# Performance work log

Hardware: AMD Instinct MI355X
Metric: run time of the kernel (lower is better)

Reference implementation:

```python
import jax, jax.numpy as jnp
import numpy as np

NEG_SLOPE = 0.01  # torch nn.LeakyReLU default


def setup_inputs() -> dict:
    key = jax.random.key(0)
    k1, k2, k3, k4 = jax.random.split(key, 4)
    B, N, d = 256, 64, 64
    embeddings = jax.random.normal(k1, (B, N, d), dtype=jnp.float32)
    # nn.Linear(em_dim, em_dim): weight [d, d] (out, in), bias [d]
    w_W = jax.random.normal(k2, (d, d), dtype=jnp.float32) / np.sqrt(d)
    w_b = jax.random.normal(k3, (d,), dtype=jnp.float32) * 0.01
    # nn.Linear(em_dim, 1): weight [1, d] -> stored as [d], bias [1]
    a_W = jax.random.normal(k4, (d,), dtype=jnp.float32) / np.sqrt(d)
    a_b = jnp.zeros((1,), dtype=jnp.float32)
    return {"embeddings": embeddings, "w_W": w_W, "w_b": w_b, "a_W": a_W, "a_b": a_b}


def reference(embeddings, w_W, w_b, a_W, a_b):
    # pairwise elementwise product: value[b,i,j,d] = emb[b,i,d] * emb[b,j,d]
    value = embeddings[:, :, None, :] * embeddings[:, None, :, :]  # [B,N,N,d]
    # small linear d->d (torch Linear: x @ W.T + b)
    qk = jnp.einsum('bijd,ed->bije', value, w_W) + w_b
    qk = jnp.where(qk >= 0, qk, NEG_SLOPE * qk)  # LeakyReLU
    # dropout is identity in eval mode
    logits = jnp.einsum('bijd,d->bij', qk, a_W) + a_b[0]  # linear d->1, squeeze
    alphas = jax.nn.softmax(logits, axis=-1)[..., None]  # [B,N,N,1]
    return alphas, value
```

## Files before the change

kernel.cpp:

```cpp
#include <hip/hip_runtime.h>

typedef __attribute__((ext_vector_type(8))) short short8;
typedef __attribute__((ext_vector_type(4))) float floatx4;
typedef __attribute__((ext_vector_type(4))) int   intx4;

#define NEG_SLOPE 0.01f

__device__ __forceinline__ short f2bf(float f) {
    unsigned u = __float_as_uint(f);
    unsigned r = (u + 0x7FFFu + ((u >> 16) & 1u)) >> 16;
    return (short)r;
}

__device__ __forceinline__ int pack2(float x, float y) {
    return (int)(unsigned short)f2bf(x) | ((int)(unsigned short)f2bf(y) << 16);
}

__global__ __launch_bounds__(512, 4)
void afm_kernel(const float* __restrict__ emb,
                const float* __restrict__ wW,
                const float* __restrict__ wb,
                const float* __restrict__ aW,
                float* __restrict__ aOut,
                float* __restrict__ vOut) {
    __shared__ __align__(16) float sEf[64][68];
    __shared__ __align__(16) float sW [64][68];
    __shared__ __align__(16) short sEb[64][72];
    __shared__ __align__(16) float sei[8][64];
    __shared__ __align__(16) float swb[64];
    __shared__ __align__(16) float saw[64];
    __shared__ __align__(16) float slog[8][64];

    const int tid   = threadIdx.x;
    const int lane  = tid & 63;
    const int w     = tid >> 6;
    const int blk   = blockIdx.x;
    const int b     = blk >> 3;
    const int iBase = (blk & 7) << 3;
    const int i     = iBase + w;

    const float* embB = emb + (size_t)b * 4096;

    {
        int row = tid >> 3;
        int c0  = (tid & 7) << 3;
        const float* src = embB + row * 64 + c0;
        float4 a0 = *(const float4*)(src);
        float4 a1 = *(const float4*)(src + 4);
        *(float4*)&sEf[row][c0]     = a0;
        *(float4*)&sEf[row][c0 + 4] = a1;
        intx4 q;
        q[0] = pack2(a0.x, a0.y); q[1] = pack2(a0.z, a0.w);
        q[2] = pack2(a1.x, a1.y); q[3] = pack2(a1.z, a1.w);
        *(intx4*)&sEb[row][c0] = q;

        const float* wsrc = wW + row * 64 + c0;
        float4 b0 = *(const float4*)(wsrc);
        float4 b1 = *(const float4*)(wsrc + 4);
        *(float4*)&sW[row][c0]     = b0;
        *(float4*)&sW[row][c0 + 4] = b1;

        sei[w][lane] = embB[i * 64 + lane];
        if (tid < 64)        swb[tid]       = wb[tid];
        else if (tid < 128)  saw[tid - 64]  = aW[tid - 64];
    }
    __syncthreads();

    {
        float* base = vOut + ((size_t)(b * 64 + i) << 12);
        const int joff = lane >> 4;
        const int d0   = (lane & 15) << 2;
        float4 ei = *(float4*)&sei[w][d0];
        #pragma unroll
        for (int c = 0; c < 16; ++c) {
            int j = (c << 2) + joff;
            float4 ej = *(float4*)&sEf[j][d0];
            floatx4 v;
            v[0] = ei.x * ej.x; v[1] = ei.y * ej.y;
            v[2] = ei.z * ej.z; v[3] = ei.w * ej.w;
            __builtin_nontemporal_store(v, (floatx4*)(base + (c << 8) + (lane << 2)));
        }
    }

    const int lo = lane & 15, hi = lane >> 4;

    short8 bf[2][4];
    #pragma unroll
    for (int kt = 0; kt < 2; ++kt) {
        const int d0 = kt * 32 + hi * 8;
        float4 ei0 = *(float4*)&sei[w][d0];
        float4 ei1 = *(float4*)&sei[w][d0 + 4];
        #pragma unroll
        for (int et = 0; et < 4; ++et) {
            int e = et * 16 + lo;
            float4 w0 = *(float4*)&sW[e][d0];
            float4 w1 = *(float4*)&sW[e][d0 + 4];
            short8 t;
            t[0] = f2bf(w0.x * ei0.x); t[1] = f2bf(w0.y * ei0.y);
            t[2] = f2bf(w0.z * ei0.z); t[3] = f2bf(w0.w * ei0.w);
            t[4] = f2bf(w1.x * ei1.x); t[5] = f2bf(w1.y * ei1.y);
            t[6] = f2bf(w1.z * ei1.z); t[7] = f2bf(w1.w * ei1.w);
            bf[kt][et] = t;
        }
    }

    float wbv[4], awv[4];
    #pragma unroll
    for (int et = 0; et < 4; ++et) {
        int e = et * 16 + lo;
        wbv[et] = swb[e];
        awv[et] = saw[e];
    }

    float lg[16];
    #pragma unroll
    for (int jt = 0; jt < 4; ++jt) {
        floatx4 acc[4];
        #pragma unroll
        for (int et = 0; et < 4; ++et)
            acc[et] = (floatx4){0.f, 0.f, 0.f, 0.f};
        #pragma unroll
        for (int kt = 0; kt < 2; ++kt) {
            short8 af = *(short8*)&sEb[jt * 16 + lo][kt * 32 + hi * 8];
            #pragma unroll
            for (int et = 0; et < 4; ++et)
                acc[et] = __builtin_amdgcn_mfma_f32_16x16x32_bf16(
                    af, bf[kt][et], acc[et], 0, 0, 0);
        }
        #pragma unroll
        for (int r = 0; r < 4; ++r) {
            float p = 0.f;
            #pragma unroll
            for (int et = 0; et < 4; ++et) {
                float x = acc[et][r] + wbv[et];
                x = fmaxf(x, NEG_SLOPE * x);
                p += awv[et] * x;
            }
            p += __shfl_xor(p, 1);
            p += __shfl_xor(p, 2);
            p += __shfl_xor(p, 4);
            p += __shfl_xor(p, 8);
            lg[jt * 4 + r] = p;
        }
    }

    float m = lg[0];
    #pragma unroll
    for (int k = 1; k < 16; ++k) m = fmaxf(m, lg[k]);
    m = fmaxf(m, __shfl_xor(m, 16));
    m = fmaxf(m, __shfl_xor(m, 32));

    float ex[16];
    float s = 0.f;
    #pragma unroll
    for (int k = 0; k < 16; ++k) { ex[k] = __expf(lg[k] - m); s += ex[k]; }
    s += __shfl_xor(s, 16);
    s += __shfl_xor(s, 32);
    float inv = 1.f / s;

    if (lo == 0) {
        #pragma unroll
        for (int jt = 0; jt < 4; ++jt)
            #pragma unroll
            for (int r = 0; r < 4; ++r)
                slog[w][jt * 16 + hi * 4 + r] = ex[jt * 4 + r] * inv;
    }
    __syncthreads();
    aOut[((size_t)(b * 64 + i) << 6) + lane] = slog[w][lane];
}

extern "C" void kernel_launch(void* const* d_in, const int* in_sizes, int n_in,
                              void* d_out, int out_size, void* d_ws, size_t ws_size,
                              hipStream_t stream) {
    const float* emb = (const float*)d_in[0];
    const float* wW  = (const float*)d_in[1];
    const float* wb  = (const float*)d_in[2];
    const float* aW  = (const float*)d_in[3];
    float* aOut = (float*)d_out;
    float* vOut = aOut + (size_t)256 * 64 * 64;
    afm_kernel<<<2048, 512, 0, stream>>>(emb, wW, wb, aW, aOut, vOut);
}
```

Measured before the change: 279.5 us.

## Interleave value stores with MFMA logit compute and drop weight staging in LDS

Moves the value-tensor nontemporal stores into the same loop as the MFMA logit computation, so each group of four store chunks is followed by one jt tile of matrix work, overlapping the write stream with compute. Weight, bias and attention vectors are now read directly from global memory instead of being staged through shared memory, which shrinks the LDS footprint. The final block-wide __syncthreads is replaced with a wave barrier, since each wave only reads its own slog row. Logits pass through shared memory so the softmax can read them back, at the cost of an extra LDS round trip and redundant per-thread global weight loads.

```diff
diff --git a/kernel.cpp b/kernel.cpp
--- a/kernel.cpp
+++ b/kernel.cpp
@@ -24,11 +24,8 @@
                 float* __restrict__ aOut,
                 float* __restrict__ vOut) {
     __shared__ __align__(16) float sEf[64][68];
-    __shared__ __align__(16) float sW [64][68];
     __shared__ __align__(16) short sEb[64][72];
     __shared__ __align__(16) float sei[8][64];
-    __shared__ __align__(16) float swb[64];
-    __shared__ __align__(16) float saw[64];
     __shared__ __align__(16) float slog[8][64];
 
     const int tid   = threadIdx.x;
@@ -54,33 +51,9 @@
         q[2] = pack2(a1.x, a1.y); q[3] = pack2(a1.z, a1.w);
         *(intx4*)&sEb[row][c0] = q;
 
-        const float* wsrc = wW + row * 64 + c0;
-        float4 b0 = *(const float4*)(wsrc);
-        float4 b1 = *(const float4*)(wsrc + 4);
-        *(float4*)&sW[row][c0]     = b0;
-        *(float4*)&sW[row][c0 + 4] = b1;
-
         sei[w][lane] = embB[i * 64 + lane];
-        if (tid < 64)        swb[tid]       = wb[tid];
-        else if (tid < 128)  saw[tid - 64]  = aW[tid - 64];
     }
     __syncthreads();
-
-    {
-        float* base = vOut + ((size_t)(b * 64 + i) << 12);
-        const int joff = lane >> 4;
-        const int d0   = (lane & 15) << 2;
-        float4 ei = *(float4*)&sei[w][d0];
-        #pragma unroll
-        for (int c = 0; c < 16; ++c) {
-            int j = (c << 2) + joff;
-            float4 ej = *(float4*)&sEf[j][d0];
-            floatx4 v;
-            v[0] = ei.x * ej.x; v[1] = ei.y * ej.y;
-            v[2] = ei.z * ej.z; v[3] = ei.w * ej.w;
-            __builtin_nontemporal_store(v, (floatx4*)(base + (c << 8) + (lane << 2)));
-        }
-    }
 
     const int lo = lane & 15, hi = lane >> 4;
 
@@ -92,9 +65,9 @@
         float4 ei1 = *(float4*)&sei[w][d0 + 4];
         #pragma unroll
         for (int et = 0; et < 4; ++et) {
-            int e = et * 16 + lo;
-            float4 w0 = *(float4*)&sW[e][d0];
-            float4 w1 = *(float4*)&sW[e][d0 + 4];
+            const float* wp = wW + (et * 16 + lo) * 64 + d0;
+            float4 w0 = *(const float4*)(wp);
+            float4 w1 = *(const float4*)(wp + 4);
             short8 t;
             t[0] = f2bf(w0.x * ei0.x); t[1] = f2bf(w0.y * ei0.y);
             t[2] = f2bf(w0.z * ei0.z); t[3] = f2bf(w0.w * ei0.w);
@@ -103,57 +76,85 @@
             bf[kt][et] = t;
         }
     }
-
     float wbv[4], awv[4];
     #pragma unroll
     for (int et = 0; et < 4; ++et) {
-        int e = et * 16 + lo;
-        wbv[et] = swb[e];
-        awv[et] = saw[e];
+        wbv[et] = wb[et * 16 + lo];
+        awv[et] = aW[et * 16 + lo];
     }
 
-    float lg[16];
+    float* base = vOut + ((size_t)(b * 64 + i) << 12);
+    const int joff = lane >> 4;
+    const int d0v  = (lane & 15) << 2;
+    floatx4 eiv = *(floatx4*)&sei[w][d0v];
+
     #pragma unroll
-    for (int jt = 0; jt < 4; ++jt) {
-        floatx4 acc[4];
-        #pragma unroll
-        for (int et = 0; et < 4; ++et)
-            acc[et] = (floatx4){0.f, 0.f, 0.f, 0.f};
-        #pragma unroll
-        for (int kt = 0; kt < 2; ++kt) {
-            short8 af = *(short8*)&sEb[jt * 16 + lo][kt * 32 + hi * 8];
+    for (int c = 0; c < 16; ++c) {
+        int j = (c << 2) + joff;
+        floatx4 ej = *(floatx4*)&sEf[j][d0v];
+        floatx4 v  = eiv * ej;
+        __builtin_nontemporal_store(v, (floatx4*)(base + (c << 8) + (lane << 2)));
+
+        if ((c & 3) == 3) {
+            const int jt = c >> 2;
+            short8 af0 = *(short8*)&sEb[jt * 16 + lo][hi * 8];
+            short8 af1 = *(short8*)&sEb[jt * 16 + lo][32 + hi * 8];
+            floatx4 acc[4];
+            #pragma unroll
+            for (int et = 0; et < 4; ++et)
+                acc[et] = (floatx4){0.f, 0.f, 0.f, 0.f};
             #pragma unroll
             for (int et = 0; et < 4; ++et)
                 acc[et] = __builtin_amdgcn_mfma_f32_16x16x32_bf16(
-                    af, bf[kt][et], acc[et], 0, 0, 0);
-        }
-        #pragma unroll
-        for (int r = 0; r < 4; ++r) {
-            float p = 0.f;
+                    af0, bf[0][et], acc[et], 0, 0, 0);
             #pragma unroll
-            for (int et = 0; et < 4; ++et) {
-                float x = acc[et][r] + wbv[et];
-                x = fmaxf(x, NEG_SLOPE * x);
-                p += awv[et] * x;
+            for (int et = 0; et < 4; ++et)
+                acc[et] = __builtin_amdgcn_mfma_f32_16x16x32_bf16(
+                    af1, bf[1][et], acc[et], 0, 0, 0);
+            #pragma unroll
+            for (int r = 0; r < 4; ++r) {
+                float p = 0.f;
+                #pragma unroll
+                for (int et = 0; et < 4; ++et) {
+                    float x = acc[et][r] + wbv[et];
+                    x = fmaxf(x, NEG_SLOPE * x);
+                    p += awv[et] * x;
+                }
+                p += __shfl_xor(p, 1);
+                p += __shfl_xor(p, 2);
+                p += __shfl_xor(p, 4);
+                p += __shfl_xor(p, 8);
+                if (lo == 0)
+                    slog[w][jt * 16 + hi * 4 + r] = p;
             }
-            p += __shfl_xor(p, 1);
-            p += __shfl_xor(p, 2);
-            p += __shfl_xor(p, 4);
-            p += __shfl_xor(p, 8);
-            lg[jt * 4 + r] = p;
+            __builtin_amdgcn_sched_barrier(0);
         }
     }
 
-    float m = lg[0];
+    __builtin_amdgcn_wave_barrier();
+    floatx4 lgv[4];
     #pragma unroll
-    for (int k = 1; k < 16; ++k) m = fmaxf(m, lg[k]);
+    for (int jt = 0; jt < 4; ++jt)
+        lgv[jt] = *(floatx4*)&slog[w][jt * 16 + hi * 4];
+
+    float m = lgv[0][0];
+    #pragma unroll
+    for (int jt = 0; jt < 4; ++jt)
+        #pragma unroll
+        for (int r = 0; r < 4; ++r) m = fmaxf(m, lgv[jt][r]);
     m = fmaxf(m, __shfl_xor(m, 16));
     m = fmaxf(m, __shfl_xor(m, 32));
 
     float ex[16];
     float s = 0.f;
     #pragma unroll
-    for (int k = 0; k < 16; ++k) { ex[k] = __expf(lg[k] - m); s += ex[k]; }
+    for (int jt = 0; jt < 4; ++jt)
+        #pragma unroll
+        for (int r = 0; r < 4; ++r) {
+            float e = __expf(lgv[jt][r] - m);
+            ex[jt * 4 + r] = e;
+            s += e;
+        }
     s += __shfl_xor(s, 16);
     s += __shfl_xor(s, 32);
     float inv = 1.f / s;
@@ -165,7 +166,7 @@
             for (int r = 0; r < 4; ++r)
                 slog[w][jt * 16 + hi * 4 + r] = ex[jt * 4 + r] * inv;
     }
-    __syncthreads();
+    __builtin_amdgcn_wave_barrier();
     aOut[((size_t)(b * 64 + i) << 6) + lane] = slog[w][lane];
 }
 
```

Result: slower. 298.0 us (+6.6%).
